# Performance work log

Measured on AMD Instinct MI355X. Metric: run time of the kernel, lower is better.

Reference implementation:

```python
import jax, jax.numpy as jnp
import numpy as np
from jax import lax

B, C, W = 16, 64, 125000  # batch, EEG channels, raw samples
KH, KW, SW, OC = 3, 2500, 1250, 32


def setup_inputs() -> dict:
    key = jax.random.key(0)
    ks = jax.random.split(key, 10)
    inp = {
        "x": jax.random.normal(ks[0], (B, 1, C, W), dtype=jnp.float32),
        # Conv2d(1->32, kernel=(3,2500))
        "conv_w": jax.random.normal(ks[1], (OC, 1, KH, KW), dtype=jnp.float32) * 0.02,
        "conv_b": jax.random.normal(ks[2], (OC,), dtype=jnp.float32) * 0.02,
        # Conv2d(32->1, kernel=(1,1))
        "conv2_w": jax.random.normal(ks[3], (1, OC, 1, 1), dtype=jnp.float32) * 0.1,
        "conv2_b": jax.random.normal(ks[4], (1,), dtype=jnp.float32) * 0.1,
        # nn.RNN(input_size=1, hidden_size=1): scalar weights
        "w_ih": jax.random.normal(ks[5], (1, 1), dtype=jnp.float32),
        "w_hh": jax.random.normal(ks[6], (1, 1), dtype=jnp.float32),
        "b_ih": jax.random.normal(ks[7], (1,), dtype=jnp.float32) * 0.1,
        "b_hh": jax.random.normal(ks[8], (1,), dtype=jnp.float32) * 0.1,
        # torch.rand(num_layers=1, B, 1) hidden init, reused for every row i
        "h0": jax.random.uniform(ks[9], (1, B, 1), dtype=jnp.float32),
    }
    return inp


def reference(x, conv_w, conv_b, conv2_w, conv2_b, w_ih, w_hh, b_ih, b_hh, h0):
    # F.pad(x, (0,0,1,1), 'replicate'): pad channel (height) dim by 1 each side
    xp = jnp.pad(x, ((0, 0), (0, 0), (1, 1), (0, 0)), mode="edge")
    # conv + relu -> [B, 32, C, T]
    y = lax.conv_general_dilated(
        xp, conv_w, window_strides=(1, SW), padding="VALID",
        dimension_numbers=("NCHW", "OIHW", "NCHW"))
    y = jax.nn.relu(y + conv_b[None, :, None, None])
    # 1x1 conv 32->1 + relu -> [B, C, T]
    z = jnp.einsum("bohw,o->bhw", y, conv2_w[0, :, 0, 0]) + conv2_b[0]
    z = jax.nn.relu(z)
    # Elman RNN with scalar weights, scanned over T; carry is [B, C]
    wih, whh = w_ih[0, 0], w_hh[0, 0]
    bias = b_ih[0] + b_hh[0]
    h_init = jnp.broadcast_to(h0[0, :, 0][:, None], z.shape[:2])  # [B, C]

    def step(h, xt):  # xt: [B, C]
        h = jnp.tanh(wih * xt + whh * h + bias)
        return h, None

    xs = jnp.moveaxis(z, -1, 0)  # [T, B, C]
    h_final, _ = lax.scan(step, h_init, xs)
    return jax.nn.sigmoid(h_final)  # [B, C]
```

## Files before the change

### kernel.cpp

```cpp
#include <hip/hip_runtime.h>
#include <math.h>

#define B_ 16
#define C_ 64
#define J_ 100
#define T_ 99
#define KW_ 1250
#define KP_ 1280
#define N_ 192
#define M_ (B_*C_*J_)
#define BM 128
#define BK 32
#define NCHUNK 40

typedef __attribute__((ext_vector_type(8))) _Float16 half8;
typedef __attribute__((ext_vector_type(4))) float f32x4;
typedef __attribute__((ext_vector_type(2), aligned(8))) float f32x2;

#define GLD_LDS16(gp, lp) \
    __builtin_amdgcn_global_load_lds((const __attribute__((address_space(1))) void*)(gp), \
                                     (__attribute__((address_space(3))) void*)(lp), 16, 0, 0)

__global__ __launch_bounds__(256) void wconv_kernel(const float* __restrict__ cw,
                                                    _Float16* __restrict__ wh)
{
    int n = blockIdx.x;
    int o = n / 6, rem = n - o * 6, kh = rem >> 1, hf = rem & 1;
    const float* src = cw + o * 7500 + kh * 2500 + hf * 1250;
    for (int k = threadIdx.x; k < KP_; k += 256)
        wh[n * KP_ + k] = (k < KW_) ? (_Float16)src[k] : (_Float16)0.f;
}

__global__ __launch_bounds__(256, 2) void gemm_kernel(const float* __restrict__ x,
                                                      const _Float16* __restrict__ wh,
                                                      float* __restrict__ P)
{
    __shared__ __align__(16) _Float16 sm[2][(BM + N_) * BK];

    const int tid  = threadIdx.x;
    const int bm0  = blockIdx.x * BM;
    const int lane = tid & 63;
    const int wave = tid >> 6;
    const int wm   = (wave & 1) * 64;
    const int wn   = (wave >> 1) * 96;
    const int l15  = lane & 15;
    const int lq   = lane >> 4;

    const float* ap[2]; int koff[2]; int adst[2];
#pragma unroll
    for (int u = 0; u < 2; u++) {
        int q = u * 256 + tid;
        int r = q >> 2, p = q & 3;
        ap[u]   = x + (size_t)(bm0 + r) * KW_ + p * 8;
        koff[u] = p * 8;
        adst[u] = q * 8;
    }
    const _Float16* bp[3]; int bdst[3];
#pragma unroll
    for (int i = 0; i < 3; i++) {
        int qb = (i * 4 + wave) * 64 + lane;
        int n = qb >> 2, p = qb & 3;
        bp[i]   = wh + n * KP_ + p * 8;
        bdst[i] = (i * 4 + wave) * 512;
    }

    f32x4 acc[4][6];
#pragma unroll
    for (int mi = 0; mi < 4; mi++)
#pragma unroll
        for (int ni = 0; ni < 6; ni++) acc[mi][ni] = (f32x4){0.f, 0.f, 0.f, 0.f};

    f32x2 areg[2][2][4];
#define LOADA(k0, slot)                                                        \
    do {                                                                       \
        _Pragma("unroll") for (int u = 0; u < 2; u++)                          \
        _Pragma("unroll") for (int j = 0; j < 4; j++) {                        \
            int k = (k0) + koff[u] + j * 2;            \
            areg[slot][u][j] = (k + 2 <= KW_)                                  \
                ? *(const f32x2*)(ap[u] + (k0) + j * 2)                        \
                : (f32x2){0.f, 0.f};                                           \
        }                                                                      \
    } while (0)

    LOADA(0, 0);
    LOADA(BK, 1);
    {
        _Float16* Bb = &sm[0][BM * BK];
#pragma unroll
        for (int i = 0; i < 3; i++) GLD_LDS16(bp[i], Bb + bdst[i]);
    }

    for (int ck = 0; ck < NCHUNK; ck++) {
        const int slot = ck & 1;
        _Float16* Ab = &sm[slot][0];
        _Float16* Bb = &sm[slot][BM * BK];

#pragma unroll
        for (int u = 0; u < 2; u++) {
            half8 h;
#pragma unroll
            for (int j = 0; j < 4; j++) {
                h[2 * j]     = (_Float16)areg[slot][u][j].x;
                h[2 * j + 1] = (_Float16)areg[slot][u][j].y;
            }
            *(half8*)(Ab + adst[u]) = h;
        }

        __syncthreads();

        if (ck + 2 < NCHUNK) LOADA((ck + 2) * BK, slot);
        if (ck + 1 < NCHUNK) {
            _Float16* Bn = &sm[slot ^ 1][BM * BK];
            const int k1 = (ck + 1) * BK;
#pragma unroll
            for (int i = 0; i < 3; i++) GLD_LDS16(bp[i] + k1, Bn + bdst[i]);
        }

        half8 afr[4], bfr[6];
#pragma unroll
        for (int mi = 0; mi < 4; mi++)
            afr[mi] = *(const half8*)(Ab + (wm + mi * 16 + l15) * BK + lq * 8);
#pragma unroll
        for (int ni = 0; ni < 6; ni++)
            bfr[ni] = *(const half8*)(Bb + (wn + ni * 16 + l15) * BK + lq * 8);
#pragma unroll
        for (int mi = 0; mi < 4; mi++)
#pragma unroll
            for (int ni = 0; ni < 6; ni++)
                acc[mi][ni] = __builtin_amdgcn_mfma_f32_16x16x32_f16(
                    afr[mi], bfr[ni], acc[mi][ni], 0, 0, 0);
    }

#pragma unroll
    for (int mi = 0; mi < 4; mi++) {
        int mrow = bm0 + wm + mi * 16 + lq * 4;
#pragma unroll
        for (int ni = 0; ni < 6; ni++) {
            int n = wn + ni * 16 + l15;
#pragma unroll
            for (int r2 = 0; r2 < 4; r2++)
                P[(size_t)(mrow + r2) * N_ + n] = acc[mi][ni][r2];
        }
    }
#undef LOADA
}

__global__ __launch_bounds__(256) void combine_kernel(const float* __restrict__ P,
                                                      const float* __restrict__ conv_b,
                                                      const float* __restrict__ c2w,
                                                      const float* __restrict__ c2b,
                                                      float* __restrict__ z)
{
    __shared__ float Pl[64][196];
    __shared__ float red[4][64];
    const int t   = blockIdx.x;
    const int b   = blockIdx.y;
    const int tid = threadIdx.x;
    const int c   = tid & 63;
    const int og  = tid >> 6;

    float v[8];
#pragma unroll
    for (int o = 0; o < 8; o++) v[o] = conv_b[og * 8 + o];

    for (int hf = 0; hf < 2; hf++) {
        const int j = t + hf;
        __syncthreads();
        for (int idx = tid; idx < 64 * N_; idx += 256) {
            int r = idx / N_, nn = idx - r * N_;
            Pl[r][nn] = P[((size_t)((b * 64 + r) * J_ + j)) * N_ + nn];
        }
        __syncthreads();
#pragma unroll
        for (int kh = 0; kh < 3; kh++) {
            int r = c + kh - 1;
            r = r < 0 ? 0 : (r > 63 ? 63 : r);
#pragma unroll
            for (int o = 0; o < 8; o++)
                v[o] += Pl[r][(og * 8 + o) * 6 + kh * 2 + hf];
        }
    }

    float part = 0.f;
#pragma unroll
    for (int o = 0; o < 8; o++) part += fmaxf(v[o], 0.f) * c2w[og * 8 + o];
    red[og][c] = part;
    __syncthreads();
    if (og == 0) {
        float zz = red[0][c] + red[1][c] + red[2][c] + red[3][c] + c2b[0];
        z[(size_t)(b * 64 + c) * T_ + t] = fmaxf(zz, 0.f);
    }
}

__global__ __launch_bounds__(256) void rnn_kernel(const float* __restrict__ z,
                                                  const float* __restrict__ w_ih,
                                                  const float* __restrict__ w_hh,
                                                  const float* __restrict__ b_ih,
                                                  const float* __restrict__ b_hh,
                                                  const float* __restrict__ h0,
                                                  float* __restrict__ out)
{
    int g = blockIdx.x * 256 + threadIdx.x;
    if (g >= B_ * C_) return;
    int b = g >> 6;
    const float wih  = w_ih[0];
    const float whh  = w_hh[0];
    const float bias = b_ih[0] + b_hh[0];
    float h = h0[b];
    const float* zp = z + (size_t)g * T_;
    for (int t = 0; t < T_; t++)
        h = tanhf(fmaf(wih, zp[t], fmaf(whh, h, bias)));
    out[g] = 1.f / (1.f + expf(-h));
}

extern "C" void kernel_launch(void* const* d_in, const int* in_sizes, int n_in,
                              void* d_out, int out_size, void* d_ws, size_t ws_size,
                              hipStream_t stream)
{
    const float* x   = (const float*)d_in[0];
    const float* cw  = (const float*)d_in[1];
    const float* cb  = (const float*)d_in[2];
    const float* c2w = (const float*)d_in[3];
    const float* c2b = (const float*)d_in[4];
    const float* wih = (const float*)d_in[5];
    const float* whh = (const float*)d_in[6];
    const float* bih = (const float*)d_in[7];
    const float* bhh = (const float*)d_in[8];
    const float* h0  = (const float*)d_in[9];
    float* out = (float*)d_out;

    const size_t whbytes = (size_t)N_ * KP_ * sizeof(_Float16);
    const size_t pbytes  = (size_t)M_ * N_ * sizeof(float);
    const size_t zbytes  = (size_t)B_ * C_ * T_ * sizeof(float);

    if (ws_size < whbytes + pbytes + zbytes) return;

    _Float16* wh = (_Float16*)d_ws;
    float* P = (float*)((char*)d_ws + whbytes);
    float* z = (float*)((char*)d_ws + whbytes + pbytes);

    wconv_kernel<<<N_, 256, 0, stream>>>(cw, wh);
    gemm_kernel<<<M_ / BM, 256, 0, stream>>>(x, wh, P);
    combine_kernel<<<dim3(T_, B_), 256, 0, stream>>>(P, cb, c2w, c2b, z);
    rnn_kernel<<<4, 256, 0, stream>>>(z, wih, whh, bih, bhh, h0, out);
}
```

Measured before the change: 840.4 us.

## Store GEMM partials in fp16 and reorder rows for contiguous combine reads

The GEMM now writes its partial-product matrix P in fp16 instead of fp32, halving the intermediate write and read traffic. Rows are permuted to (b, j, c) order so the combine kernel reads one contiguous block per (b, j) with 16-byte vector loads instead of strided per-channel rows. z is stored time-major so RNN threads read coalesced. Rounding the partial sums to fp16 adds some precision risk.

```diff
diff --git a/kernel.cpp b/kernel.cpp
--- a/kernel.cpp
+++ b/kernel.cpp
@@ -33,7 +33,7 @@
 
 __global__ __launch_bounds__(256, 2) void gemm_kernel(const float* __restrict__ x,
                                                       const _Float16* __restrict__ wh,
-                                                      float* __restrict__ P)
+                                                      _Float16* __restrict__ P)
 {
     __shared__ __align__(16) _Float16 sm[2][(BM + N_) * BK];
 
@@ -49,9 +49,14 @@
     const float* ap[2]; int koff[2]; int adst[2];
 #pragma unroll
     for (int u = 0; u < 2; u++) {
-        int q = u * 256 + tid;
-        int r = q >> 2, p = q & 3;
-        ap[u]   = x + (size_t)(bm0 + r) * KW_ + p * 8;
+        int q  = u * 256 + tid;
+        int rl = q >> 2, p = q & 3;
+        int gr = bm0 + rl;
+        int b  = gr / 6400;
+        int j  = (gr - b * 6400) >> 6;
+        int c  = gr & 63;
+        long xrow = (long)(b * 64 + c) * 100 + j;
+        ap[u]   = x + xrow * KW_ + p * 8;
         koff[u] = p * 8;
         adst[u] = q * 8;
     }
@@ -74,10 +79,10 @@
 #define LOADA(k0, slot)                                                        \
     do {                                                                       \
         _Pragma("unroll") for (int u = 0; u < 2; u++)                          \
-        _Pragma("unroll") for (int j = 0; j < 4; j++) {                        \
-            int k = (k0) + koff[u] + j * 2;            \
-            areg[slot][u][j] = (k + 2 <= KW_)                                  \
-                ? *(const f32x2*)(ap[u] + (k0) + j * 2)                        \
+        _Pragma("unroll") for (int j2 = 0; j2 < 4; j2++) {                     \
+            int k = (k0) + koff[u] + j2 * 2;           \
+            areg[slot][u][j2] = (k + 2 <= KW_)                                 \
+                ? *(const f32x2*)(ap[u] + (k0) + j2 * 2)                       \
                 : (f32x2){0.f, 0.f};                                           \
         }                                                                      \
     } while (0)
@@ -99,9 +104,9 @@
         for (int u = 0; u < 2; u++) {
             half8 h;
 #pragma unroll
-            for (int j = 0; j < 4; j++) {
-                h[2 * j]     = (_Float16)areg[slot][u][j].x;
-                h[2 * j + 1] = (_Float16)areg[slot][u][j].y;
+            for (int j2 = 0; j2 < 4; j2++) {
+                h[2 * j2]     = (_Float16)areg[slot][u][j2].x;
+                h[2 * j2 + 1] = (_Float16)areg[slot][u][j2].y;
             }
             *(half8*)(Ab + adst[u]) = h;
         }
@@ -139,19 +144,19 @@
             int n = wn + ni * 16 + l15;
 #pragma unroll
             for (int r2 = 0; r2 < 4; r2++)
-                P[(size_t)(mrow + r2) * N_ + n] = acc[mi][ni][r2];
+                P[(size_t)(mrow + r2) * N_ + n] = (_Float16)acc[mi][ni][r2];
         }
     }
 #undef LOADA
 }
 
-__global__ __launch_bounds__(256) void combine_kernel(const float* __restrict__ P,
+__global__ __launch_bounds__(256) void combine_kernel(const _Float16* __restrict__ P,
                                                       const float* __restrict__ conv_b,
                                                       const float* __restrict__ c2w,
                                                       const float* __restrict__ c2b,
                                                       float* __restrict__ z)
 {
-    __shared__ float Pl[64][196];
+    __shared__ float Pl[64][193];
     __shared__ float red[4][64];
     const int t   = blockIdx.x;
     const int b   = blockIdx.y;
@@ -165,10 +170,16 @@
 
     for (int hf = 0; hf < 2; hf++) {
         const int j = t + hf;
+        const _Float16* Pb = P + (size_t)((b * 100 + j) * 64) * N_;
         __syncthreads();
-        for (int idx = tid; idx < 64 * N_; idx += 256) {
-            int r = idx / N_, nn = idx - r * N_;
-            Pl[r][nn] = P[((size_t)((b * 64 + r) * J_ + j)) * N_ + nn];
+#pragma unroll
+        for (int i = 0; i < 6; i++) {
+            int e   = i * 256 + tid;
+            half8 h = *(const half8*)(Pb + e * 8);
+            int row = e / 24;
+            int col = (e - row * 24) * 8;
+#pragma unroll
+            for (int u = 0; u < 8; u++) Pl[row][col + u] = (float)h[u];
         }
         __syncthreads();
 #pragma unroll
@@ -188,7 +199,7 @@
     __syncthreads();
     if (og == 0) {
         float zz = red[0][c] + red[1][c] + red[2][c] + red[3][c] + c2b[0];
-        z[(size_t)(b * 64 + c) * T_ + t] = fmaxf(zz, 0.f);
+        z[t * (B_ * C_) + b * 64 + c] = fmaxf(zz, 0.f);
     }
 }
 
@@ -207,9 +218,8 @@
     const float whh  = w_hh[0];
     const float bias = b_ih[0] + b_hh[0];
     float h = h0[b];
-    const float* zp = z + (size_t)g * T_;
     for (int t = 0; t < T_; t++)
-        h = tanhf(fmaf(wih, zp[t], fmaf(whh, h, bias)));
+        h = tanhf(fmaf(wih, z[t * (B_ * C_) + g], fmaf(whh, h, bias)));
     out[g] = 1.f / (1.f + expf(-h));
 }
 
@@ -230,14 +240,14 @@
     float* out = (float*)d_out;
 
     const size_t whbytes = (size_t)N_ * KP_ * sizeof(_Float16);
-    const size_t pbytes  = (size_t)M_ * N_ * sizeof(float);
+    const size_t pbytes  = (size_t)M_ * N_ * sizeof(_Float16);
     const size_t zbytes  = (size_t)B_ * C_ * T_ * sizeof(float);
 
     if (ws_size < whbytes + pbytes + zbytes) return;
 
     _Float16* wh = (_Float16*)d_ws;
-    float* P = (float*)((char*)d_ws + whbytes);
-    float* z = (float*)((char*)d_ws + whbytes + pbytes);
+    _Float16* P  = (_Float16*)((char*)d_ws + whbytes);
+    float*    z  = (float*)((char*)d_ws + whbytes + pbytes);
 
     wconv_kernel<<<N_, 256, 0, stream>>>(cw, wh);
     gemm_kernel<<<M_ / BM, 256, 0, stream>>>(x, wh, P);
```

New measurement: 819.5 us. 1.03x faster.
